# Performance work log

Measured on AMD Instinct MI355X. Metric: run time of the kernel, lower is better.

## Reference

```python
import jax, jax.numpy as jnp
import numpy as np
from jax import lax

B, C, H, W = 8, 64, 256, 256
LENGTH = 9
REDUCTION = 8
HIDDEN = max(8, C // REDUCTION)


def _conv(x, w, b, pad):
    # x: [B,Cin,H,W], w: [Cout,Cin,kh,kw]
    y = lax.conv_general_dilated(x, w, (1, 1), [(pad, pad), (pad, pad)],
                                 dimension_numbers=('NCHW', 'OIHW', 'NCHW'))
    return y + b[None, :, None, None]


def _bilinear(img, cy, cx):
    # img: [B,C,H,W]; cy,cx: [B,H,W] float coords already clipped to [0, size-1]
    # Matches F.grid_sample(mode='bilinear', padding_mode='border', align_corners=True)
    Hh, Ww = img.shape[2], img.shape[3]
    y0 = jnp.floor(cy)
    x0 = jnp.floor(cx)
    wy = (cy - y0)[:, None]  # [B,1,H,W]
    wx = (cx - x0)[:, None]
    y0i = y0.astype(jnp.int32)
    x0i = x0.astype(jnp.int32)
    y1i = jnp.minimum(y0i + 1, Hh - 1)
    x1i = jnp.minimum(x0i + 1, Ww - 1)

    def g(im, iy, ix):
        return im[:, iy, ix]  # [C,H,W]

    gather = jax.vmap(g)
    v00 = gather(img, y0i, x0i)
    v01 = gather(img, y0i, x1i)
    v10 = gather(img, y1i, x0i)
    v11 = gather(img, y1i, x1i)
    return (v00 * (1 - wy) * (1 - wx) + v01 * (1 - wy) * wx
            + v10 * wy * (1 - wx) + v11 * wy * wx)


def _oriented_pool(x, vx, vy, length):
    # x: [B,C,H,W]; vx,vy: [B,1,H,W] direction fields
    _, _, Hh, Ww = x.shape
    yy = jnp.arange(Hh, dtype=x.dtype)[None, :, None]  # [1,H,1]
    xx = jnp.arange(Ww, dtype=x.dtype)[None, None, :]  # [1,1,W]
    half = length // 2
    offsets = jnp.arange(-half, half + 1, dtype=x.dtype)
    vx2 = vx[:, 0]  # [B,H,W]
    vy2 = vy[:, 0]

    def step(acc, t):
        cy = jnp.clip(yy + t * vy2, 0.0, Hh - 1)
        cx = jnp.clip(xx + t * vx2, 0.0, Ww - 1)
        return acc + _bilinear(x, cy, cx), None

    acc, _ = lax.scan(step, jnp.zeros_like(x), offsets)
    return acc / length


def setup_inputs() -> dict:
    key = jax.random.key(0)
    ks = jax.random.split(key, 5)

    def he(k, shape, fan_in):
        return jax.random.normal(k, shape, jnp.float32) * np.float32(1.0 / np.sqrt(fan_in))

    return {
        'x': jax.random.normal(ks[0], (B, C, H, W), jnp.float32),
        'w3': he(ks[1], (HIDDEN, C, 3, 3), C * 9),
        'b3': jnp.zeros((HIDDEN,), jnp.float32),
        'w1': he(ks[2], (1, HIDDEN, 1, 1), HIDDEN),
        'b1': jnp.zeros((1,), jnp.float32),
        'wr': he(ks[3], (HIDDEN, 2 * C, 1, 1), 2 * C),
        'br': jnp.zeros((HIDDEN,), jnp.float32),
        'we': he(ks[4], (2 * C, HIDDEN, 1, 1), HIDDEN),
        'be': jnp.zeros((2 * C,), jnp.float32),
    }


def reference(x, w3, b3, w1, b1, wr, br, we, be):
    theta = jnp.pi * jax.nn.sigmoid(_conv(jax.nn.relu(_conv(x, w3, b3, 1)), w1, b1, 0))  # [B,1,H,W]
    cos_t = jnp.cos(theta)
    sin_t = jnp.sin(theta)
    tan_feat = _oriented_pool(x, cos_t, sin_t, LENGTH)
    nor_feat = _oriented_pool(x, -sin_t, cos_t, LENGTH)
    context = jnp.concatenate([tan_feat, nor_feat], axis=1)  # [B,2C,H,W]
    w = jax.nn.sigmoid(_conv(jax.nn.relu(_conv(context, wr, br, 0)), we, be, 0))  # [B,2C,H,W]
    alpha_tan, alpha_norm = jnp.split(w, 2, axis=1)
    return (alpha_tan + alpha_norm) * x
```

## Files before the change

kernel.cpp:

```cpp
#include <hip/hip_runtime.h>
#include <math.h>

#define Bb 8
#define Cc 64
#define Hh 256
#define Ww 256
#define HID 8
#define PLANE (Hh*Ww)

typedef _Float16 f16x2 __attribute__((ext_vector_type(2)));

static __device__ __forceinline__ f16x2 u2h(unsigned int u) {
    return __builtin_bit_cast(f16x2, u);
}
static __device__ __forceinline__ unsigned int h2u(f16x2 h) {
    return __builtin_bit_cast(unsigned int, h);
}

#define TPH 13
#define TPW 74
#define TPP 75
#define TPN (TPH*TPW)

__global__ __launch_bounds__(256, 4) void fused_kernel(
    const float* __restrict__ x,
    const float* __restrict__ w3, const float* __restrict__ b3,
    const float* __restrict__ w1, const float* __restrict__ b1,
    const float* __restrict__ wr, const float* __restrict__ br,
    const float* __restrict__ we, const float* __restrict__ be,
    float* __restrict__ out)
{
    __shared__ uint2 tile[TPH * TPP];
    const int tid = threadIdx.x;
    const int tx = tid & 63;
    const int ty = tid >> 6;
    const int xx = blockIdx.x * 64 + tx;
    const int yy = blockIdx.y * 4 + ty;
    const int b  = blockIdx.z;
    const int row0 = blockIdx.y * 4 - 4;
    const int col0 = blockIdx.x * 64 - 4;

    int goff[4], loff[4];
    #pragma unroll
    for (int k = 0; k < 4; k++) {
        int i = tid + k * 256;
        i = (i < TPN) ? i : (TPN - 1);
        const int r  = i / TPW;
        const int cc = i - r * TPW;
        const int gy = min(max(row0 + r, 0), Hh - 1);
        const int gx = min(max(col0 + cc, 0), Ww - 1);
        goff[k] = gy * Ww + gx;
        loff[k] = r * TPP + cc;
    }
    #pragma unroll
    for (int k = 0; k < 4; k++)
        asm volatile("" : "+v"(goff[k]), "+v"(loff[k]));

    const int lcen = (ty + 4) * TPP + (tx + 4);
    const float* xb = x + (size_t)b * Cc * PLANE;

    const bool interior = (blockIdx.y > 0) && (blockIdx.y < (Hh/4 - 1)) &&
                          (blockIdx.x > 0) && (blockIdx.x < (Ww/64 - 1));
    float mk[9];
    #pragma unroll
    for (int dy = 0; dy < 3; dy++)
        #pragma unroll
        for (int dx = 0; dx < 3; dx++) {
            const int gy = yy + dy - 1, gx = xx + dx - 1;
            mk[dy*3+dx] = (gy >= 0 && gy < Hh && gx >= 0 && gx < Ww) ? 1.f : 0.f;
        }

    float rv[4][4];
    #pragma unroll
    for (int k = 0; k < 4; k++)
        #pragma unroll
        for (int q = 0; q < 4; q++)
            rv[k][q] = xb[goff[k] + (size_t)q * PLANE];

    float acc[HID];
    #pragma unroll
    for (int h = 0; h < HID; h++) acc[h] = 0.f;

    for (int st = 0; st < Cc / 4; st++) {
        __syncthreads();
        #pragma unroll
        for (int k = 0; k < 4; k++)
            tile[loff[k]] = make_uint2(
                h2u((f16x2){(_Float16)rv[k][0], (_Float16)rv[k][1]}),
                h2u((f16x2){(_Float16)rv[k][2], (_Float16)rv[k][3]}));
        {
            const int nst = (st + 1 < Cc / 4) ? st + 1 : 0;
            const float* xn = xb + (size_t)nst * 4 * PLANE;
            #pragma unroll
            for (int k = 0; k < 4; k++)
                #pragma unroll
                for (int q = 0; q < 4; q++)
                    rv[k][q] = xn[goff[k] + (size_t)q * PLANE];
        }
        __syncthreads();

        float va[9][4];
        #pragma unroll
        for (int dy = 0; dy < 3; dy++)
            #pragma unroll
            for (int dx = 0; dx < 3; dx++) {
                const uint2 cv = tile[lcen + (dy - 1) * TPP + (dx - 1)];
                const f16x2 lo = u2h(cv.x), hi = u2h(cv.y);
                const int k = dy * 3 + dx;
                va[k][0] = (float)lo.x; va[k][1] = (float)lo.y;
                va[k][2] = (float)hi.x; va[k][3] = (float)hi.y;
            }
        if (!interior) {
            #pragma unroll
            for (int k = 0; k < 9; k++)
                #pragma unroll
                for (int q = 0; q < 4; q++) va[k][q] *= mk[k];
        }
        #pragma unroll
        for (int h = 0; h < HID; h++) {
            const float* wk = w3 + (size_t)(h * Cc + st * 4) * 9;
            float a = acc[h];
            #pragma unroll
            for (int q = 0; q < 4; q++)
                #pragma unroll
                for (int k = 0; k < 9; k++)
                    a = fmaf(wk[q * 9 + k], va[k][q], a);
            acc[h] = a;
        }
    }

    float z = b1[0];
    #pragma unroll
    for (int h = 0; h < HID; h++) {
        float hr = acc[h] + b3[h];
        hr = hr > 0.f ? hr : 0.f;
        z = fmaf(w1[h], hr, z);
    }
    const float theta = 3.14159265358979f / (1.f + __expf(-z));
    float vy, vx;
    __sincosf(theta, &vy, &vx);

    int off[16];
    unsigned int wxp[16], wyp[16];
    #pragma unroll
    for (int s = 0; s < 9; s++) {
        if (s == 4) continue;
        const int j = (s < 4) ? s : s - 1;
        const float t = (float)(s - 4);
        {
            float cy = fminf(fmaxf((float)yy + t * vy, 0.f), (float)(Hh - 1));
            float cx = fminf(fmaxf((float)xx + t * vx, 0.f), (float)(Ww - 1));
            int y0 = min((int)cy, Hh - 2);
            int x0 = min((int)cx, Ww - 2);
            off[j] = (y0 - row0) * TPP + (x0 - col0);
            const float wy = cy - (float)y0, wxx = cx - (float)x0;
            wxp[j] = h2u((f16x2){(_Float16)wxx, (_Float16)wxx});
            wyp[j] = h2u((f16x2){(_Float16)wy,  (_Float16)wy});
        }
        {
            float cy = fminf(fmaxf((float)yy + t * vx, 0.f), (float)(Hh - 1));
            float cx = fminf(fmaxf((float)xx - t * vy, 0.f), (float)(Ww - 1));
            int y0 = min((int)cy, Hh - 2);
            int x0 = min((int)cx, Ww - 2);
            off[8 + j] = (y0 - row0) * TPP + (x0 - col0);
            const float wy = cy - (float)y0, wxx = cx - (float)x0;
            wxp[8 + j] = h2u((f16x2){(_Float16)wxx, (_Float16)wxx});
            wyp[8 + j] = h2u((f16x2){(_Float16)wy,  (_Float16)wy});
        }
    }
    #pragma unroll
    for (int s = 0; s < 16; s++)
        asm volatile("" : "+v"(off[s]), "+v"(wxp[s]), "+v"(wyp[s]));

    float hid[HID];
    #pragma unroll
    for (int h = 0; h < HID; h++) hid[h] = br[h];

    for (int cp = 0; cp < Cc / 4; cp++) {
        __syncthreads();
        #pragma unroll
        for (int k = 0; k < 4; k++)
            tile[loff[k]] = make_uint2(
                h2u((f16x2){(_Float16)rv[k][0], (_Float16)rv[k][1]}),
                h2u((f16x2){(_Float16)rv[k][2], (_Float16)rv[k][3]}));
        if (cp + 1 < Cc / 4) {
            const float* xn = xb + (size_t)(cp + 1) * 4 * PLANE;
            #pragma unroll
            for (int k = 0; k < 4; k++)
                #pragma unroll
                for (int q = 0; q < 4; q++)
                    rv[k][q] = xn[goff[k] + (size_t)q * PLANE];
        }
        __syncthreads();

        const uint2 cc = tile[lcen];
        const f16x2 clo = u2h(cc.x), chi = u2h(cc.y);
        float tac[4], nac[4];
        tac[0] = nac[0] = (float)clo.x;
        tac[1] = nac[1] = (float)clo.y;
        tac[2] = nac[2] = (float)chi.x;
        tac[3] = nac[3] = (float)chi.y;

        #pragma unroll
        for (int s = 0; s < 16; s++) {
            const int o = off[s];
            const uint2 c00 = tile[o];
            const uint2 c01 = tile[o + 1];
            const uint2 c10 = tile[o + TPP];
            const uint2 c11 = tile[o + TPP + 1];
            const f16x2 wxh = u2h(wxp[s]);
            const f16x2 wyh = u2h(wyp[s]);
            const f16x2 a00 = u2h(c00.x), a01 = u2h(c01.x);
            const f16x2 a10 = u2h(c10.x), a11 = u2h(c11.x);
            const f16x2 e00 = u2h(c00.y), e01 = u2h(c01.y);
            const f16x2 e10 = u2h(c10.y), e11 = u2h(c11.y);
            const f16x2 t0  = a00 + wxh * (a01 - a00);
            const f16x2 b0v = a10 + wxh * (a11 - a10);
            const f16x2 t1  = e00 + wxh * (e01 - e00);
            const f16x2 b1v = e10 + wxh * (e11 - e10);
            const f16x2 v0  = t0 + wyh * (b0v - t0);
            const f16x2 v1  = t1 + wyh * (b1v - t1);
            const float s0 = (float)v0.x, s1 = (float)v0.y;
            const float s2 = (float)v1.x, s3 = (float)v1.y;
            if (s < 8) { tac[0]+=s0; tac[1]+=s1; tac[2]+=s2; tac[3]+=s3; }
            else       { nac[0]+=s0; nac[1]+=s1; nac[2]+=s2; nac[3]+=s3; }
        }
        const int c = 4 * cp;
        #pragma unroll
        for (int q = 0; q < 4; q++) {
            const float tq = tac[q] * (1.f / 9.f);
            const float nq = nac[q] * (1.f / 9.f);
            #pragma unroll
            for (int h = 0; h < HID; h++) {
                float a = hid[h];
                a = fmaf(wr[h * 128 + c + q],      tq, a);
                a = fmaf(wr[h * 128 + 64 + c + q], nq, a);
                hid[h] = a;
            }
        }
    }

    #pragma unroll
    for (int h = 0; h < HID; h++) hid[h] = fmaxf(hid[h], 0.f);

    const int pix = yy * Ww + xx;
    for (int c = 0; c < Cc; c++) {
        float z1 = be[c];
        float z2 = be[c + 64];
        #pragma unroll
        for (int h = 0; h < HID; h++) {
            z1 = fmaf(we[c * 8 + h],        hid[h], z1);
            z2 = fmaf(we[(c + 64) * 8 + h], hid[h], z2);
        }
        const float a1 = 1.f / (1.f + __expf(-z1));
        const float a2 = 1.f / (1.f + __expf(-z2));
        const float xv = xb[c * PLANE + pix];
        out[(size_t)(b * Cc + c) * PLANE + pix] = (a1 + a2) * xv;
    }
}

extern "C" void kernel_launch(void* const* d_in, const int* in_sizes, int n_in,
                              void* d_out, int out_size, void* d_ws, size_t ws_size,
                              hipStream_t stream) {
    const float* x  = (const float*)d_in[0];
    const float* w3 = (const float*)d_in[1];
    const float* b3 = (const float*)d_in[2];
    const float* w1 = (const float*)d_in[3];
    const float* b1 = (const float*)d_in[4];
    const float* wr = (const float*)d_in[5];
    const float* br = (const float*)d_in[6];
    const float* we = (const float*)d_in[7];
    const float* be = (const float*)d_in[8];
    float* out = (float*)d_out;

    dim3 grid(Ww / 64, Hh / 4, Bb);
    dim3 block(256);
    fused_kernel<<<grid, block, 0, stream>>>(x, w3, b3, w1, b1,
                                             wr, br, we, be, out);
}
```

Before: 499.2 us.

## Double-buffer the LDS tile to halve barriers and use packed RTZ fp16 conversion

```diff
diff --git a/kernel.cpp b/kernel.cpp
--- a/kernel.cpp
+++ b/kernel.cpp
@@ -13,8 +13,8 @@
 static __device__ __forceinline__ f16x2 u2h(unsigned int u) {
     return __builtin_bit_cast(f16x2, u);
 }
-static __device__ __forceinline__ unsigned int h2u(f16x2 h) {
-    return __builtin_bit_cast(unsigned int, h);
+static __device__ __forceinline__ unsigned int pkrtz(float a, float b) {
+    return __builtin_bit_cast(unsigned int, __builtin_amdgcn_cvt_pkrtz(a, b));
 }
 
 #define TPH 13
@@ -22,7 +22,7 @@
 #define TPP 75
 #define TPN (TPH*TPW)
 
-__global__ __launch_bounds__(256, 4) void fused_kernel(
+__global__ __launch_bounds__(256, 3) void fused_kernel(
     const float* __restrict__ x,
     const float* __restrict__ w3, const float* __restrict__ b3,
     const float* __restrict__ w1, const float* __restrict__ b1,
@@ -30,7 +30,7 @@
     const float* __restrict__ we, const float* __restrict__ be,
     float* __restrict__ out)
 {
-    __shared__ uint2 tile[TPH * TPP];
+    __shared__ uint2 buf[2][TPH * TPP];
     const int tid = threadIdx.x;
     const int tx = tid & 63;
     const int ty = tid >> 6;
@@ -58,53 +58,55 @@
 
     const int lcen = (ty + 4) * TPP + (tx + 4);
     const float* xb = x + (size_t)b * Cc * PLANE;
-
     const bool interior = (blockIdx.y > 0) && (blockIdx.y < (Hh/4 - 1)) &&
                           (blockIdx.x > 0) && (blockIdx.x < (Ww/64 - 1));
-    float mk[9];
-    #pragma unroll
-    for (int dy = 0; dy < 3; dy++)
-        #pragma unroll
-        for (int dx = 0; dx < 3; dx++) {
-            const int gy = yy + dy - 1, gx = xx + dx - 1;
-            mk[dy*3+dx] = (gy >= 0 && gy < Hh && gx >= 0 && gx < Ww) ? 1.f : 0.f;
-        }
-
-    float rv[4][4];
+
+    float rvf[4][4];
     #pragma unroll
     for (int k = 0; k < 4; k++)
         #pragma unroll
         for (int q = 0; q < 4; q++)
-            rv[k][q] = xb[goff[k] + (size_t)q * PLANE];
+            rvf[k][q] = xb[goff[k] + (size_t)q * PLANE];
+    #pragma unroll
+    for (int k = 0; k < 4; k++)
+        buf[0][loff[k]] = make_uint2(pkrtz(rvf[k][0], rvf[k][1]),
+                                     pkrtz(rvf[k][2], rvf[k][3]));
+    {
+        const float* xn = xb + (size_t)4 * PLANE;
+        #pragma unroll
+        for (int k = 0; k < 4; k++)
+            #pragma unroll
+            for (int q = 0; q < 4; q++)
+                rvf[k][q] = xn[goff[k] + (size_t)q * PLANE];
+    }
+    __syncthreads();
 
     float acc[HID];
     #pragma unroll
     for (int h = 0; h < HID; h++) acc[h] = 0.f;
 
-    for (int st = 0; st < Cc / 4; st++) {
-        __syncthreads();
+    for (int g = 0; g < 16; g++) {
+        const int pr = g & 1, nx = pr ^ 1;
         #pragma unroll
         for (int k = 0; k < 4; k++)
-            tile[loff[k]] = make_uint2(
-                h2u((f16x2){(_Float16)rv[k][0], (_Float16)rv[k][1]}),
-                h2u((f16x2){(_Float16)rv[k][2], (_Float16)rv[k][3]}));
+            buf[nx][loff[k]] = make_uint2(pkrtz(rvf[k][0], rvf[k][1]),
+                                          pkrtz(rvf[k][2], rvf[k][3]));
         {
-            const int nst = (st + 1 < Cc / 4) ? st + 1 : 0;
-            const float* xn = xb + (size_t)nst * 4 * PLANE;
+            const int s2 = g + 2;
+            const int cb = (s2 < 16 ? s2 : s2 - 16) * 4;
+            const float* xn = xb + (size_t)cb * PLANE;
             #pragma unroll
             for (int k = 0; k < 4; k++)
                 #pragma unroll
                 for (int q = 0; q < 4; q++)
-                    rv[k][q] = xn[goff[k] + (size_t)q * PLANE];
-        }
-        __syncthreads();
-
+                    rvf[k][q] = xn[goff[k] + (size_t)q * PLANE];
+        }
         float va[9][4];
         #pragma unroll
         for (int dy = 0; dy < 3; dy++)
             #pragma unroll
             for (int dx = 0; dx < 3; dx++) {
-                const uint2 cv = tile[lcen + (dy - 1) * TPP + (dx - 1)];
+                const uint2 cv = buf[pr][lcen + (dy - 1) * TPP + (dx - 1)];
                 const f16x2 lo = u2h(cv.x), hi = u2h(cv.y);
                 const int k = dy * 3 + dx;
                 va[k][0] = (float)lo.x; va[k][1] = (float)lo.y;
@@ -112,13 +114,19 @@
             }
         if (!interior) {
             #pragma unroll
-            for (int k = 0; k < 9; k++)
-                #pragma unroll
-                for (int q = 0; q < 4; q++) va[k][q] *= mk[k];
+            for (int dy = 0; dy < 3; dy++)
+                #pragma unroll
+                for (int dx = 0; dx < 3; dx++) {
+                    const int gy = yy + dy - 1, gx = xx + dx - 1;
+                    const float m = (gy >= 0 && gy < Hh &&
+                                     gx >= 0 && gx < Ww) ? 1.f : 0.f;
+                    #pragma unroll
+                    for (int q = 0; q < 4; q++) va[dy*3+dx][q] *= m;
+                }
         }
         #pragma unroll
         for (int h = 0; h < HID; h++) {
-            const float* wk = w3 + (size_t)(h * Cc + st * 4) * 9;
+            const float* wk = w3 + (size_t)(h * Cc + g * 4) * 9;
             float a = acc[h];
             #pragma unroll
             for (int q = 0; q < 4; q++)
@@ -127,6 +135,7 @@
                     a = fmaf(wk[q * 9 + k], va[k][q], a);
             acc[h] = a;
         }
+        __syncthreads();
     }
 
     float z = b1[0];
@@ -154,8 +163,8 @@
             int x0 = min((int)cx, Ww - 2);
             off[j] = (y0 - row0) * TPP + (x0 - col0);
             const float wy = cy - (float)y0, wxx = cx - (float)x0;
-            wxp[j] = h2u((f16x2){(_Float16)wxx, (_Float16)wxx});
-            wyp[j] = h2u((f16x2){(_Float16)wy,  (_Float16)wy});
+            wxp[j] = pkrtz(wxx, wxx);
+            wyp[j] = pkrtz(wy,  wy);
         }
         {
             float cy = fminf(fmaxf((float)yy + t * vx, 0.f), (float)(Hh - 1));
@@ -164,8 +173,8 @@
             int x0 = min((int)cx, Ww - 2);
             off[8 + j] = (y0 - row0) * TPP + (x0 - col0);
             const float wy = cy - (float)y0, wxx = cx - (float)x0;
-            wxp[8 + j] = h2u((f16x2){(_Float16)wxx, (_Float16)wxx});
-            wyp[8 + j] = h2u((f16x2){(_Float16)wy,  (_Float16)wy});
+            wxp[8 + j] = pkrtz(wxx, wxx);
+            wyp[8 + j] = pkrtz(wy,  wy);
         }
     }
     #pragma unroll
@@ -176,24 +185,25 @@
     #pragma unroll
     for (int h = 0; h < HID; h++) hid[h] = br[h];
 
-    for (int cp = 0; cp < Cc / 4; cp++) {
-        __syncthreads();
-        #pragma unroll
-        for (int k = 0; k < 4; k++)
-            tile[loff[k]] = make_uint2(
-                h2u((f16x2){(_Float16)rv[k][0], (_Float16)rv[k][1]}),
-                h2u((f16x2){(_Float16)rv[k][2], (_Float16)rv[k][3]}));
-        if (cp + 1 < Cc / 4) {
-            const float* xn = xb + (size_t)(cp + 1) * 4 * PLANE;
+    for (int g = 16; g < 32; g++) {
+        const int pr = g & 1, nx = pr ^ 1;
+        if (g < 31) {
             #pragma unroll
             for (int k = 0; k < 4; k++)
-                #pragma unroll
-                for (int q = 0; q < 4; q++)
-                    rv[k][q] = xn[goff[k] + (size_t)q * PLANE];
-        }
-        __syncthreads();
-
-        const uint2 cc = tile[lcen];
+                buf[nx][loff[k]] = make_uint2(pkrtz(rvf[k][0], rvf[k][1]),
+                                              pkrtz(rvf[k][2], rvf[k][3]));
+            if (g < 30) {
+                const int cb = (g + 2 - 16) * 4;
+                const float* xn = xb + (size_t)cb * PLANE;
+                #pragma unroll
+                for (int k = 0; k < 4; k++)
+                    #pragma unroll
+                    for (int q = 0; q < 4; q++)
+                        rvf[k][q] = xn[goff[k] + (size_t)q * PLANE];
+            }
+        }
+
+        const uint2 cc = buf[pr][lcen];
         const f16x2 clo = u2h(cc.x), chi = u2h(cc.y);
         float tac[4], nac[4];
         tac[0] = nac[0] = (float)clo.x;
@@ -204,10 +214,10 @@
         #pragma unroll
         for (int s = 0; s < 16; s++) {
             const int o = off[s];
-            const uint2 c00 = tile[o];
-            const uint2 c01 = tile[o + 1];
-            const uint2 c10 = tile[o + TPP];
-            const uint2 c11 = tile[o + TPP + 1];
+            const uint2 c00 = buf[pr][o];
+            const uint2 c01 = buf[pr][o + 1];
+            const uint2 c10 = buf[pr][o + TPP];
+            const uint2 c11 = buf[pr][o + TPP + 1];
             const f16x2 wxh = u2h(wxp[s]);
             const f16x2 wyh = u2h(wyp[s]);
             const f16x2 a00 = u2h(c00.x), a01 = u2h(c01.x);
@@ -225,7 +235,7 @@
             if (s < 8) { tac[0]+=s0; tac[1]+=s1; tac[2]+=s2; tac[3]+=s3; }
             else       { nac[0]+=s0; nac[1]+=s1; nac[2]+=s2; nac[3]+=s3; }
         }
-        const int c = 4 * cp;
+        const int c = 4 * (g - 16);
         #pragma unroll
         for (int q = 0; q < 4; q++) {
             const float tq = tac[q] * (1.f / 9.f);
@@ -238,6 +248,7 @@
                 hid[h] = a;
             }
         }
+        if (g < 31) __syncthreads();
     }
 
     #pragma unroll
```

New measurement: 477.2 us. 4.4% less time.
